# Optimization experiments

Measured on AMD Instinct MI355X. Metric: run time of the kernel, lower is better.

The kernel has to match this reference:

```python
import jax, jax.numpy as jnp
import numpy as np

DIM_BODY = 10
DIM_OBJECT = 15
NB_OBJECTS = 3
FIRST_INDS = np.array([0,1,2,3,4,5,6,7,8,9,10,11,12,13,15,16,17,20,21,25])
SECOND_INDS = np.array([0,1,2,3,4,5,6,7,8,9,14,18,19,22,23,24,26,27,28,29])
LOG_SIG_MIN, LOG_SIG_MAX = -20.0, 2.0


def setup_inputs() -> dict:
    key = jax.random.key(0)
    ks = jax.random.split(key, 16)
    B = 65536
    s = 0.05  # weight scale, keeps activations sane
    return {
        "obs": jax.random.normal(ks[0], (B, DIM_BODY + NB_OBJECTS * DIM_OBJECT), jnp.float32),
        "ag": jax.random.normal(ks[1], (B, 30), jnp.float32),
        "g": jax.random.normal(ks[2], (B, 30), jnp.float32),
        "phi_w1": jax.random.normal(ks[3], (80, 256), jnp.float32) * s,
        "phi_b1": jnp.zeros((256,), jnp.float32),
        "phi_w2": jax.random.normal(ks[4], (256, 256), jnp.float32) * s,
        "phi_b2": jnp.zeros((256,), jnp.float32),
        "rho_w1": jax.random.normal(ks[5], (256, 256), jnp.float32) * s,
        "rho_b1": jnp.zeros((256,), jnp.float32),
        "mean_w": jax.random.normal(ks[6], (256, 4), jnp.float32) * s,
        "mean_b": jnp.zeros((4,), jnp.float32),
        "logstd_w": jax.random.normal(ks[7], (256, 4), jnp.float32) * s,
        "logstd_b": jnp.zeros((4,), jnp.float32),
    }


def reference(obs, ag, g, phi_w1, phi_b1, phi_w2, phi_b2, rho_w1, rho_b1,
              mean_w, mean_b, logstd_w, logstd_b):
    body = obs[:, :DIM_BODY]  # [B,10]
    objs = [obs[:, DIM_BODY + DIM_OBJECT * i: DIM_BODY + DIM_OBJECT * (i + 1)]
            for i in range(NB_OBJECTS)]
    ag_f, g_f = ag[:, FIRST_INDS], g[:, FIRST_INDS]
    ag_s, g_s = ag[:, SECOND_INDS], g[:, SECOND_INDS]
    pair_inputs = []
    for i in range(NB_OBJECTS):
        for j in range(NB_OBJECTS):
            if i < j:
                pair_inputs.append(jnp.concatenate([ag_f, body, g_f, objs[i], objs[j]], axis=1))
            elif j < i:
                pair_inputs.append(jnp.concatenate([ag_s, body, g_s, objs[i], objs[j]], axis=1))
    inp = jnp.stack(pair_inputs)  # [6, B, 80]
    # shared phi MLP (2 layers, ReLU on both)
    h = jax.nn.relu(jnp.einsum('pbi,ih->pbh', inp, phi_w1) + phi_b1)
    phi = jax.nn.relu(jnp.einsum('pbh,ho->pbo', h, phi_w2) + phi_b2)
    agg = phi.sum(axis=0)  # [B, 256] sum over pairs
    # rho head
    hr = jax.nn.relu(agg @ rho_w1 + rho_b1)
    mean = hr @ mean_w + mean_b
    logstd = jnp.clip(hr @ logstd_w + logstd_b, LOG_SIG_MIN, LOG_SIG_MAX)
    return mean, logstd
```

## Files before the change

### kernel.cpp

```cpp
#include <hip/hip_runtime.h>
#include <hip/hip_bf16.h>


#define B_TOTAL 65536
#define TROWS   64
#define RSTR    136

typedef __attribute__((ext_vector_type(8))) short s8v;
typedef __attribute__((ext_vector_type(4))) float f4v;

__constant__ int c_PI[6] = {0,0,1,1,2,2};
__constant__ int c_PJ[6] = {1,2,0,2,0,1};
__constant__ int c_PF[6] = {0,0,1,0,1,1};
__constant__ int c_INV[2][30] = {
  {0,1,2,3,4,5,6,7,8,9,10,11,12,13,-1,14,15,16,-1,-1,17,18,-1,-1,-1,19,-1,-1,-1,-1},
  {0,1,2,3,4,5,6,7,8,9,-1,-1,-1,-1,10,-1,-1,-1,11,12,-1,-1,13,14,15,-1,16,17,18,19}};

__global__ void prep_weights(const float* __restrict__ phi_w1,
                             const float* __restrict__ phi_b1,
                             const float* __restrict__ phi_w2,
                             const float* __restrict__ rho_w1,
                             const float* __restrict__ mean_w,
                             const float* __restrict__ logstd_w,
                             __hip_bfloat16* __restrict__ W1P,
                             __hip_bfloat16* __restrict__ W2f,
                             __hip_bfloat16* __restrict__ W3f,
                             __hip_bfloat16* __restrict__ W4f) {
  const int i0 = blockIdx.x * blockDim.x + threadIdx.x;
  const int stride = gridDim.x * blockDim.x;
  for (int d = i0; d < 6 * 32768; d += stride) {
    int p = d >> 15, r = d & 32767;
    int j = r & 7, lane = (r >> 3) & 63, blk = r >> 9;
    int nb = blk >> 2, ks = blk & 3;
    int n = nb * 16 + (lane & 15), k = ks * 32 + (lane >> 4) * 8 + j;
    int f = c_PF[p], oi = c_PI[p], oj = c_PJ[p];
    float v = 0.0f;
    if (k < 30)       { int t = c_INV[f][k];      if (t >= 0) v = phi_w1[t * 256 + n]; }
    else if (k < 60)  { int t = c_INV[f][k - 30]; if (t >= 0) v = phi_w1[(30 + t) * 256 + n]; }
    else if (k < 70)  { v = phi_w1[(20 + k - 60) * 256 + n]; }
    else if (k < 115) { int q = (k - 70) / 15, t = (k - 70) - q * 15;
                        int c = (q == oi) ? 50 + t : (q == oj) ? 65 + t : -1;
                        if (c >= 0) v = phi_w1[c * 256 + n]; }
    else if (k == 115) v = phi_b1[n];
    W1P[d] = __float2bfloat16(v);
  }
  for (int d = i0; d < 65536; d += stride) {
    int j = d & 7, lane = (d >> 3) & 63, blk = d >> 9;
    int nb = blk >> 3, ks = blk & 7;
    int n = nb * 16 + (lane & 15), k = ks * 32 + (lane >> 4) * 8 + j;
    W2f[d] = __float2bfloat16(phi_w2[k * 256 + n]);
    W3f[d] = __float2bfloat16(rho_w1[k * 256 + n]);
  }
  for (int d = i0; d < 4096; d += stride) {
    int j = d & 7, lane = (d >> 3) & 63, ks = d >> 9;
    int n = lane & 15, k = ks * 32 + (lane >> 4) * 8 + j;
    float v = (n < 4) ? mean_w[k * 4 + n]
            : (n < 8) ? logstd_w[k * 4 + (n - 4)] : 0.0f;
    W4f[d] = __float2bfloat16(v);
  }
}

static __device__ __forceinline__ unsigned pk2(float a, float b) {
  __hip_bfloat162 h = __float22bfloat162_rn(float2{a, b});
  union { __hip_bfloat162 h2; unsigned u; } cv; cv.h2 = h;
  return cv.u;
}

__global__ __launch_bounds__(512, 2)
void actor_main(const float* __restrict__ obs, const float* __restrict__ ag,
                const float* __restrict__ g,
                const __hip_bfloat16* __restrict__ W1P,
                const __hip_bfloat16* __restrict__ W2f,
                const __hip_bfloat16* __restrict__ W3f,
                const __hip_bfloat16* __restrict__ W4f,
                const float* __restrict__ b2, const float* __restrict__ b3,
                const float* __restrict__ meanb,
                const float* __restrict__ logstdb,
                float* __restrict__ out) {
  __shared__ __align__(16) __hip_bfloat16 rawS[TROWS * RSTR];
  __shared__ __align__(16) __hip_bfloat16 Hs[4 * 8 * 512];

  const int tid  = threadIdx.x;
  const int lane = tid & 63;
  const int w    = tid >> 6;
  const int l15  = lane & 15;
  const int quad = lane >> 4;
  const int r0   = blockIdx.x * TROWS;

  float4 b2v[2], b3v[2];
#pragma unroll
  for (int i = 0; i < 2; ++i) {
    int col0 = w * 32 + i * 16 + quad * 4;
    b2v[i] = *(const float4*)&b2[col0];
    b3v[i] = *(const float4*)&b3[col0];
  }

  s8v w2f[8][2];
#pragma unroll
  for (int i = 0; i < 2; ++i)
#pragma unroll
    for (int ks = 0; ks < 8; ++ks)
      w2f[ks][i] = *(const s8v*)&W2f[(((w * 2 + i) * 8 + ks) * 512) + lane * 8];

  {
    const int row = tid >> 3;
    const int c0  = (tid & 7) * 16;
    const float* agr = ag  + (size_t)(r0 + row) * 30;
    const float* gr  = g   + (size_t)(r0 + row) * 30;
    const float* obr = obs + (size_t)(r0 + row) * 55;
#pragma unroll
    for (int cc = 0; cc < 16; ++cc) {
      int c = c0 + cc;
      float v;
      if      (c < 30)  v = agr[c];
      else if (c < 60)  v = gr[c - 30];
      else if (c < 115) v = obr[c - 60];
      else if (c == 115) v = 1.0f;
      else              v = 0.0f;
      rawS[row * RSTR + c] = __float2bfloat16(v);
    }
  }

  f4v agg[2][4];
#pragma unroll
  for (int i = 0; i < 2; ++i)
#pragma unroll
    for (int rt = 0; rt < 4; ++rt) agg[i][rt] = f4v{0.f, 0.f, 0.f, 0.f};

  const int ebase = l15 * 8 + (quad >> 1) * 128 + (quad & 1) * 4;

  __syncthreads();

#pragma unroll 1
  for (int p = 0; p < 6; ++p) {
    s8v w1f[4][2];
    {
      const __hip_bfloat16* base = W1P + p * 32768;
#pragma unroll
      for (int i = 0; i < 2; ++i)
#pragma unroll
        for (int ks = 0; ks < 4; ++ks)
          w1f[ks][i] = *(const s8v*)&base[(((w * 2 + i) * 4 + ks) * 512) + lane * 8];
    }

    f4v h[2][4];
#pragma unroll
    for (int i = 0; i < 2; ++i)
#pragma unroll
      for (int rt = 0; rt < 4; ++rt) h[i][rt] = f4v{0.f, 0.f, 0.f, 0.f};
#pragma unroll
    for (int ks = 0; ks < 4; ++ks) {
      s8v bx[4];
#pragma unroll
      for (int rt = 0; rt < 4; ++rt)
        bx[rt] = *(const s8v*)&rawS[(rt * 16 + l15) * RSTR + ks * 32 + quad * 8];
#pragma unroll
      for (int i = 0; i < 2; ++i)
#pragma unroll
        for (int rt = 0; rt < 4; ++rt)
          h[i][rt] = __builtin_amdgcn_mfma_f32_16x16x32_bf16(w1f[ks][i], bx[rt], h[i][rt], 0, 0, 0);
    }

    __syncthreads();
#pragma unroll
    for (int i = 0; i < 2; ++i)
#pragma unroll
      for (int rt = 0; rt < 4; ++rt) {
        float v0 = fmaxf(h[i][rt][0], 0.f);
        float v1 = fmaxf(h[i][rt][1], 0.f);
        float v2 = fmaxf(h[i][rt][2], 0.f);
        float v3 = fmaxf(h[i][rt][3], 0.f);
        uint2 U; U.x = pk2(v0, v1); U.y = pk2(v2, v3);
        *reinterpret_cast<uint2*>(&Hs[(rt * 8 + w) * 512 + i * 256 + ebase]) = U;
      }
    __syncthreads();

    f4v a2[2][4];
#pragma unroll
    for (int i = 0; i < 2; ++i)
#pragma unroll
      for (int rt = 0; rt < 4; ++rt) a2[i][rt] = f4v{0.f, 0.f, 0.f, 0.f};
#pragma unroll
    for (int ks = 0; ks < 8; ++ks) {
      s8v hf[4];
#pragma unroll
      for (int rt = 0; rt < 4; ++rt)
        hf[rt] = *(const s8v*)&Hs[(rt * 8 + ks) * 512 + lane * 8];
#pragma unroll
      for (int i = 0; i < 2; ++i)
#pragma unroll
        for (int rt = 0; rt < 4; ++rt)
          a2[i][rt] = __builtin_amdgcn_mfma_f32_16x16x32_bf16(w2f[ks][i], hf[rt], a2[i][rt], 0, 0, 0);
    }
#pragma unroll
    for (int i = 0; i < 2; ++i)
#pragma unroll
      for (int rt = 0; rt < 4; ++rt) {
        agg[i][rt][0] += fmaxf(a2[i][rt][0] + b2v[i].x, 0.f);
        agg[i][rt][1] += fmaxf(a2[i][rt][1] + b2v[i].y, 0.f);
        agg[i][rt][2] += fmaxf(a2[i][rt][2] + b2v[i].z, 0.f);
        agg[i][rt][3] += fmaxf(a2[i][rt][3] + b2v[i].w, 0.f);
      }
  }

  s8v w3f[8][2];
#pragma unroll
  for (int i = 0; i < 2; ++i)
#pragma unroll
    for (int ks = 0; ks < 8; ++ks)
      w3f[ks][i] = *(const s8v*)&W3f[(((w * 2 + i) * 8 + ks) * 512) + lane * 8];

  __syncthreads();
#pragma unroll
  for (int i = 0; i < 2; ++i)
#pragma unroll
    for (int rt = 0; rt < 4; ++rt) {
      uint2 U; U.x = pk2(agg[i][rt][0], agg[i][rt][1]);
      U.y = pk2(agg[i][rt][2], agg[i][rt][3]);
      *reinterpret_cast<uint2*>(&Hs[(rt * 8 + w) * 512 + i * 256 + ebase]) = U;
    }
  __syncthreads();

  f4v a3[2][4];
#pragma unroll
  for (int i = 0; i < 2; ++i)
#pragma unroll
    for (int rt = 0; rt < 4; ++rt) a3[i][rt] = f4v{0.f, 0.f, 0.f, 0.f};
#pragma unroll
  for (int ks = 0; ks < 8; ++ks) {
    s8v hf[4];
#pragma unroll
    for (int rt = 0; rt < 4; ++rt)
      hf[rt] = *(const s8v*)&Hs[(rt * 8 + ks) * 512 + lane * 8];
#pragma unroll
    for (int i = 0; i < 2; ++i)
#pragma unroll
      for (int rt = 0; rt < 4; ++rt)
        a3[i][rt] = __builtin_amdgcn_mfma_f32_16x16x32_bf16(w3f[ks][i], hf[rt], a3[i][rt], 0, 0, 0);
  }
  __syncthreads();
#pragma unroll
  for (int i = 0; i < 2; ++i)
#pragma unroll
    for (int rt = 0; rt < 4; ++rt) {
      float v0 = fmaxf(a3[i][rt][0] + b3v[i].x, 0.f);
      float v1 = fmaxf(a3[i][rt][1] + b3v[i].y, 0.f);
      float v2 = fmaxf(a3[i][rt][2] + b3v[i].z, 0.f);
      float v3 = fmaxf(a3[i][rt][3] + b3v[i].w, 0.f);
      uint2 U; U.x = pk2(v0, v1); U.y = pk2(v2, v3);
      *reinterpret_cast<uint2*>(&Hs[(rt * 8 + w) * 512 + i * 256 + ebase]) = U;
    }
  __syncthreads();

  if (w < 4) {
    f4v a4 = f4v{0.f, 0.f, 0.f, 0.f};
#pragma unroll
    for (int ks = 0; ks < 8; ++ks) {
      s8v w4 = *(const s8v*)&W4f[ks * 512 + lane * 8];
      s8v hf = *(const s8v*)&Hs[(w * 8 + ks) * 512 + lane * 8];
      a4 = __builtin_amdgcn_mfma_f32_16x16x32_bf16(w4, hf, a4, 0, 0, 0);
    }
    const int row = r0 + w * 16 + l15;
    if (quad == 0) {
      float4 mb = *(const float4*)meanb;
      float4 o;
      o.x = a4[0] + mb.x; o.y = a4[1] + mb.y;
      o.z = a4[2] + mb.z; o.w = a4[3] + mb.w;
      *reinterpret_cast<float4*>(&out[(size_t)row * 4]) = o;
    } else if (quad == 1) {
      float4 lb = *(const float4*)logstdb;
      float4 o;
      o.x = fminf(fmaxf(a4[0] + lb.x, -20.f), 2.f);
      o.y = fminf(fmaxf(a4[1] + lb.y, -20.f), 2.f);
      o.z = fminf(fmaxf(a4[2] + lb.z, -20.f), 2.f);
      o.w = fminf(fmaxf(a4[3] + lb.w, -20.f), 2.f);
      *reinterpret_cast<float4*>(&out[(size_t)B_TOTAL * 4 + (size_t)row * 4]) = o;
    }
  }
}

extern "C" void kernel_launch(void* const* d_in, const int* in_sizes, int n_in,
                              void* d_out, int out_size, void* d_ws, size_t ws_size,
                              hipStream_t stream) {
  const float* obs      = (const float*)d_in[0];
  const float* ag       = (const float*)d_in[1];
  const float* g        = (const float*)d_in[2];
  const float* phi_w1   = (const float*)d_in[3];
  const float* phi_b1   = (const float*)d_in[4];
  const float* phi_w2   = (const float*)d_in[5];
  const float* phi_b2   = (const float*)d_in[6];
  const float* rho_w1   = (const float*)d_in[7];
  const float* rho_b1   = (const float*)d_in[8];
  const float* mean_w   = (const float*)d_in[9];
  const float* mean_b   = (const float*)d_in[10];
  const float* logstd_w = (const float*)d_in[11];
  const float* logstd_b = (const float*)d_in[12];
  float* out = (float*)d_out;

  char* ws = (char*)d_ws;
  __hip_bfloat16* W1P = (__hip_bfloat16*)(ws);
  __hip_bfloat16* W2f = (__hip_bfloat16*)(ws + 393216);
  __hip_bfloat16* W3f = (__hip_bfloat16*)(ws + 393216 + 131072);
  __hip_bfloat16* W4f = (__hip_bfloat16*)(ws + 393216 + 262144);

  prep_weights<<<256, 256, 0, stream>>>(phi_w1, phi_b1, phi_w2, rho_w1,
                                        mean_w, logstd_w, W1P, W2f, W3f, W4f);
  actor_main<<<B_TOTAL / TROWS, 512, 0, stream>>>(
      obs, ag, g, W1P, W2f, W3f, W4f, phi_b2, rho_b1, mean_b, logstd_b, out);
}
```

Before: 192.7 us.

## Double-buffer hidden activations in LDS and cache layer-1 inputs in registers

The layer-1 input tile is loaded from LDS into registers once before the pair loop instead of on every pair. The raw input buffer is aliased onto a two-slot hidden-activation buffer, and pairs alternate between slots, which removes one barrier per pair iteration and one in the rho head. Layer-1 work is split per output half to limit live registers. In exchange, 64 more VGPRs hold the cached inputs, which may pressure occupancy under the 512x2 launch bounds, and correctness depends on the alternating slots never being read and written at the same time.

After: 195.8 us. About the same (+1.6%).

```diff
diff --git a/kernel.cpp b/kernel.cpp
--- a/kernel.cpp
+++ b/kernel.cpp
@@ -77,8 +77,7 @@
                 const float* __restrict__ meanb,
                 const float* __restrict__ logstdb,
                 float* __restrict__ out) {
-  __shared__ __align__(16) __hip_bfloat16 rawS[TROWS * RSTR];
-  __shared__ __align__(16) __hip_bfloat16 Hs[4 * 8 * 512];
+  __shared__ __align__(16) __hip_bfloat16 HsBuf[2][4 * 8 * 512];
 
   const int tid  = threadIdx.x;
   const int lane = tid & 63;
@@ -87,13 +86,10 @@
   const int quad = lane >> 4;
   const int r0   = blockIdx.x * TROWS;
 
-  float4 b2v[2], b3v[2];
-#pragma unroll
-  for (int i = 0; i < 2; ++i) {
-    int col0 = w * 32 + i * 16 + quad * 4;
-    b2v[i] = *(const float4*)&b2[col0];
-    b3v[i] = *(const float4*)&b3[col0];
-  }
+  float4 b2v[2];
+#pragma unroll
+  for (int i = 0; i < 2; ++i)
+    b2v[i] = *(const float4*)&b2[w * 32 + i * 16 + quad * 4];
 
   s8v w2f[8][2];
 #pragma unroll
@@ -103,6 +99,7 @@
       w2f[ks][i] = *(const s8v*)&W2f[(((w * 2 + i) * 8 + ks) * 512) + lane * 8];
 
   {
+    __hip_bfloat16* rawS = &HsBuf[0][0];
     const int row = tid >> 3;
     const int c0  = (tid & 7) * 16;
     const float* agr = ag  + (size_t)(r0 + row) * 30;
@@ -120,6 +117,18 @@
       rawS[row * RSTR + c] = __float2bfloat16(v);
     }
   }
+  __syncthreads();
+
+  s8v bxr[4][4];
+  {
+    const __hip_bfloat16* rawS = &HsBuf[0][0];
+#pragma unroll
+    for (int ks = 0; ks < 4; ++ks)
+#pragma unroll
+      for (int rt = 0; rt < 4; ++rt)
+        bxr[ks][rt] = *(const s8v*)&rawS[(rt * 16 + l15) * RSTR + ks * 32 + quad * 8];
+  }
+  __syncthreads();
 
   f4v agg[2][4];
 #pragma unroll
@@ -128,51 +137,36 @@
     for (int rt = 0; rt < 4; ++rt) agg[i][rt] = f4v{0.f, 0.f, 0.f, 0.f};
 
   const int ebase = l15 * 8 + (quad >> 1) * 128 + (quad & 1) * 4;
-
-  __syncthreads();
 
 #pragma unroll 1
   for (int p = 0; p < 6; ++p) {
-    s8v w1f[4][2];
-    {
-      const __hip_bfloat16* base = W1P + p * 32768;
-#pragma unroll
-      for (int i = 0; i < 2; ++i)
-#pragma unroll
-        for (int ks = 0; ks < 4; ++ks)
-          w1f[ks][i] = *(const s8v*)&base[(((w * 2 + i) * 4 + ks) * 512) + lane * 8];
-    }
-
-    f4v h[2][4];
-#pragma unroll
-    for (int i = 0; i < 2; ++i)
-#pragma unroll
-      for (int rt = 0; rt < 4; ++rt) h[i][rt] = f4v{0.f, 0.f, 0.f, 0.f};
-#pragma unroll
-    for (int ks = 0; ks < 4; ++ks) {
-      s8v bx[4];
-#pragma unroll
-      for (int rt = 0; rt < 4; ++rt)
-        bx[rt] = *(const s8v*)&rawS[(rt * 16 + l15) * RSTR + ks * 32 + quad * 8];
-#pragma unroll
-      for (int i = 0; i < 2; ++i)
+    __hip_bfloat16* buf = &HsBuf[p & 1][0];
+    const __hip_bfloat16* w1base = W1P + p * 32768;
+
+#pragma unroll
+    for (int i = 0; i < 2; ++i) {
+      s8v w1f[4];
+#pragma unroll
+      for (int ks = 0; ks < 4; ++ks)
+        w1f[ks] = *(const s8v*)&w1base[(((w * 2 + i) * 4 + ks) * 512) + lane * 8];
+      f4v h[4];
+#pragma unroll
+      for (int rt = 0; rt < 4; ++rt) h[rt] = f4v{0.f, 0.f, 0.f, 0.f};
+#pragma unroll
+      for (int ks = 0; ks < 4; ++ks)
 #pragma unroll
         for (int rt = 0; rt < 4; ++rt)
-          h[i][rt] = __builtin_amdgcn_mfma_f32_16x16x32_bf16(w1f[ks][i], bx[rt], h[i][rt], 0, 0, 0);
-    }
-
-    __syncthreads();
-#pragma unroll
-    for (int i = 0; i < 2; ++i)
+          h[rt] = __builtin_amdgcn_mfma_f32_16x16x32_bf16(w1f[ks], bxr[ks][rt], h[rt], 0, 0, 0);
 #pragma unroll
       for (int rt = 0; rt < 4; ++rt) {
-        float v0 = fmaxf(h[i][rt][0], 0.f);
-        float v1 = fmaxf(h[i][rt][1], 0.f);
-        float v2 = fmaxf(h[i][rt][2], 0.f);
-        float v3 = fmaxf(h[i][rt][3], 0.f);
+        float v0 = fmaxf(h[rt][0], 0.f);
+        float v1 = fmaxf(h[rt][1], 0.f);
+        float v2 = fmaxf(h[rt][2], 0.f);
+        float v3 = fmaxf(h[rt][3], 0.f);
         uint2 U; U.x = pk2(v0, v1); U.y = pk2(v2, v3);
-        *reinterpret_cast<uint2*>(&Hs[(rt * 8 + w) * 512 + i * 256 + ebase]) = U;
+        *reinterpret_cast<uint2*>(&buf[(rt * 8 + w) * 512 + i * 256 + ebase]) = U;
       }
+    }
     __syncthreads();
 
     f4v a2[2][4];
@@ -185,7 +179,7 @@
       s8v hf[4];
 #pragma unroll
       for (int rt = 0; rt < 4; ++rt)
-        hf[rt] = *(const s8v*)&Hs[(rt * 8 + ks) * 512 + lane * 8];
+        hf[rt] = *(const s8v*)&buf[(rt * 8 + ks) * 512 + lane * 8];
 #pragma unroll
       for (int i = 0; i < 2; ++i)
 #pragma unroll
@@ -209,55 +203,67 @@
 #pragma unroll
     for (int ks = 0; ks < 8; ++ks)
       w3f[ks][i] = *(const s8v*)&W3f[(((w * 2 + i) * 8 + ks) * 512) + lane * 8];
-
+  float4 b3v[2];
+#pragma unroll
+  for (int i = 0; i < 2; ++i)
+    b3v[i] = *(const float4*)&b3[w * 32 + i * 16 + quad * 4];
+
+  {
+    __hip_bfloat16* bufA = &HsBuf[0][0];
+#pragma unroll
+    for (int i = 0; i < 2; ++i)
+#pragma unroll
+      for (int rt = 0; rt < 4; ++rt) {
+        uint2 U; U.x = pk2(agg[i][rt][0], agg[i][rt][1]);
+        U.y = pk2(agg[i][rt][2], agg[i][rt][3]);
+        *reinterpret_cast<uint2*>(&bufA[(rt * 8 + w) * 512 + i * 256 + ebase]) = U;
+      }
+  }
   __syncthreads();
-#pragma unroll
-  for (int i = 0; i < 2; ++i)
-#pragma unroll
-    for (int rt = 0; rt < 4; ++rt) {
-      uint2 U; U.x = pk2(agg[i][rt][0], agg[i][rt][1]);
-      U.y = pk2(agg[i][rt][2], agg[i][rt][3]);
-      *reinterpret_cast<uint2*>(&Hs[(rt * 8 + w) * 512 + i * 256 + ebase]) = U;
-    }
+
+  f4v a3[2][4];
+#pragma unroll
+  for (int i = 0; i < 2; ++i)
+#pragma unroll
+    for (int rt = 0; rt < 4; ++rt) a3[i][rt] = f4v{0.f, 0.f, 0.f, 0.f};
+  {
+    const __hip_bfloat16* bufA = &HsBuf[0][0];
+#pragma unroll
+    for (int ks = 0; ks < 8; ++ks) {
+      s8v hf[4];
+#pragma unroll
+      for (int rt = 0; rt < 4; ++rt)
+        hf[rt] = *(const s8v*)&bufA[(rt * 8 + ks) * 512 + lane * 8];
+#pragma unroll
+      for (int i = 0; i < 2; ++i)
+#pragma unroll
+        for (int rt = 0; rt < 4; ++rt)
+          a3[i][rt] = __builtin_amdgcn_mfma_f32_16x16x32_bf16(w3f[ks][i], hf[rt], a3[i][rt], 0, 0, 0);
+    }
+  }
+  {
+    __hip_bfloat16* bufB = &HsBuf[1][0];
+#pragma unroll
+    for (int i = 0; i < 2; ++i)
+#pragma unroll
+      for (int rt = 0; rt < 4; ++rt) {
+        float v0 = fmaxf(a3[i][rt][0] + b3v[i].x, 0.f);
+        float v1 = fmaxf(a3[i][rt][1] + b3v[i].y, 0.f);
+        float v2 = fmaxf(a3[i][rt][2] + b3v[i].z, 0.f);
+        float v3 = fmaxf(a3[i][rt][3] + b3v[i].w, 0.f);
+        uint2 U; U.x = pk2(v0, v1); U.y = pk2(v2, v3);
+        *reinterpret_cast<uint2*>(&bufB[(rt * 8 + w) * 512 + i * 256 + ebase]) = U;
+      }
+  }
   __syncthreads();
 
-  f4v a3[2][4];
-#pragma unroll
-  for (int i = 0; i < 2; ++i)
-#pragma unroll
-    for (int rt = 0; rt < 4; ++rt) a3[i][rt] = f4v{0.f, 0.f, 0.f, 0.f};
-#pragma unroll
-  for (int ks = 0; ks < 8; ++ks) {
-    s8v hf[4];
-#pragma unroll
-    for (int rt = 0; rt < 4; ++rt)
-      hf[rt] = *(const s8v*)&Hs[(rt * 8 + ks) * 512 + lane * 8];
-#pragma unroll
-    for (int i = 0; i < 2; ++i)
-#pragma unroll
-      for (int rt = 0; rt < 4; ++rt)
-        a3[i][rt] = __builtin_amdgcn_mfma_f32_16x16x32_bf16(w3f[ks][i], hf[rt], a3[i][rt], 0, 0, 0);
-  }
-  __syncthreads();
-#pragma unroll
-  for (int i = 0; i < 2; ++i)
-#pragma unroll
-    for (int rt = 0; rt < 4; ++rt) {
-      float v0 = fmaxf(a3[i][rt][0] + b3v[i].x, 0.f);
-      float v1 = fmaxf(a3[i][rt][1] + b3v[i].y, 0.f);
-      float v2 = fmaxf(a3[i][rt][2] + b3v[i].z, 0.f);
-      float v3 = fmaxf(a3[i][rt][3] + b3v[i].w, 0.f);
-      uint2 U; U.x = pk2(v0, v1); U.y = pk2(v2, v3);
-      *reinterpret_cast<uint2*>(&Hs[(rt * 8 + w) * 512 + i * 256 + ebase]) = U;
-    }
-  __syncthreads();
-
   if (w < 4) {
+    const __hip_bfloat16* bufB = &HsBuf[1][0];
     f4v a4 = f4v{0.f, 0.f, 0.f, 0.f};
 #pragma unroll
     for (int ks = 0; ks < 8; ++ks) {
       s8v w4 = *(const s8v*)&W4f[ks * 512 + lane * 8];
-      s8v hf = *(const s8v*)&Hs[(w * 8 + ks) * 512 + lane * 8];
+      s8v hf = *(const s8v*)&bufB[(w * 8 + ks) * 512 + lane * 8];
       a4 = __builtin_amdgcn_mfma_f32_16x16x32_bf16(w4, hf, a4, 0, 0, 0);
     }
     const int row = r0 + w * 16 + l15;
```
